# Kernel tuning notes

Measured on AMD Instinct MI355X. Metric: run time of the kernel, lower is better.

The kernel has to match this reference:

```python
import jax, jax.numpy as jnp
import numpy as np
import math

T = 2048; HID = 2048; H = 16; KV = 8; G = H // KV; D = 128
GH = 128; BS = 64; NB = T // BS
EPS = 1e-6; RATIO = 0.2; SCALE = 1.0 / math.sqrt(D)


def _rope_tables(length, dim, theta=1000000.0):
    inv = 1.0 / (theta ** (np.arange(0, dim, 2, dtype=np.float32) / dim))
    f = np.outer(np.arange(length, dtype=np.float32), inv)
    emb = np.concatenate([f, f], axis=-1)
    return jnp.asarray(np.cos(emb)), jnp.asarray(np.sin(emb))


def _rot_half(x):
    d = x.shape[-1] // 2
    return jnp.concatenate([-x[..., d:], x[..., :d]], axis=-1)


def _apply_rope(x, cos, sin):
    # x: [T, nH, D], cos/sin: [T, D] broadcast over head dim
    return x * cos[:, None, :] + _rot_half(x) * sin[:, None, :]


def _rmsnorm(x, w, eps=EPS):
    xf = x.astype(jnp.float32)
    v = jnp.mean(xf * xf, axis=-1, keepdims=True)
    return (w * (xf * jax.lax.rsqrt(v + eps))).astype(x.dtype)


def setup_inputs() -> dict:
    key = jax.random.key(0)
    ks = jax.random.split(key, 8)
    s = 0.02
    hidden_states = jax.random.normal(ks[0], (T, HID), jnp.float32)
    Wq = jax.random.normal(ks[1], (HID, H * D), jnp.float32) * s
    Wk = jax.random.normal(ks[2], (HID, KV * D), jnp.float32) * s
    Wv = jax.random.normal(ks[3], (HID, KV * D), jnp.float32) * s
    Wo = jax.random.normal(ks[4], (H * D, HID), jnp.float32) * s
    q_norm_w = jnp.ones((D,), jnp.float32)
    k_norm_w = jnp.ones((D,), jnp.float32)
    gate_wq = jax.random.normal(ks[5], (D, GH), jnp.float32) * s
    gate_wk = jax.random.normal(ks[6], (D, GH), jnp.float32) * s
    cos, sin = _rope_tables(T, D)
    cos_gq, sin_gq = _rope_tables(T, GH)
    cos_blk, sin_blk = _rope_tables(NB, GH)
    # causal block mask: query t may attend to key block j iff j <= t // BS
    block_attention_mask = (jnp.arange(T)[:, None] // BS) >= jnp.arange(NB)[None, :]
    return dict(hidden_states=hidden_states, Wq=Wq, Wk=Wk, Wv=Wv, Wo=Wo,
                q_norm_w=q_norm_w, k_norm_w=k_norm_w, gate_wq=gate_wq, gate_wk=gate_wk,
                cos=cos, sin=sin, cos_gq=cos_gq, sin_gq=sin_gq,
                cos_blk=cos_blk, sin_blk=sin_blk,
                block_attention_mask=block_attention_mask)


def reference(hidden_states, Wq, Wk, Wv, Wo, q_norm_w, k_norm_w, gate_wq, gate_wk,
              cos, sin, cos_gq, sin_gq, cos_blk, sin_blk, block_attention_mask):
    q = (hidden_states @ Wq).reshape(T, H, D)
    k = (hidden_states @ Wk).reshape(T, KV, D)
    v = (hidden_states @ Wv).reshape(T, KV, D)
    q = _rmsnorm(q, q_norm_w)
    k = _rmsnorm(k, k_norm_w)

    # ---- gate network on un-roped q/k: q-head avg-pool to KV heads, k avg-pool per block ----
    q_pool = q.reshape(T, KV, G, D).mean(axis=2)            # [T, KV, D]
    gq = _apply_rope(q_pool @ gate_wq, cos_gq, sin_gq)      # [T, KV, GH]
    k_blk = k.reshape(NB, BS, KV, D).mean(axis=1)           # [NB, KV, D]
    gk = _apply_rope(k_blk @ gate_wk, cos_blk, sin_blk)     # [NB, KV, GH]
    gate_scores = jnp.einsum('tkg,nkg->ktn', gq, gk) / math.sqrt(GH)  # [KV, T, NB]
    predict_mask = jnp.where(block_attention_mask[None], gate_scores, -1e9)

    # ---- main attention (RoPE + GQA causal softmax attention) ----
    qr = _apply_rope(q, cos, sin)
    kr = _apply_rope(k, cos, sin)
    kr_rep = jnp.repeat(kr, G, axis=1)                      # [T, H, D]
    v_rep = jnp.repeat(v, G, axis=1)
    logits = jnp.einsum('thd,shd->hts', qr, kr_rep) * SCALE  # [H, T, T]
    causal = jnp.tril(jnp.ones((T, T), bool))
    logits = jnp.where(causal[None], logits, -jnp.inf)
    probs = jax.nn.softmax(logits, axis=-1)
    attn_output = jnp.einsum('hts,shd->thd', probs, v_rep).reshape(T, H * D) @ Wo

    # ---- pooled ground-truth block mask: attention mass per key block ----
    pooled = probs.reshape(H, T, NB, BS).sum(axis=-1)        # [H, T, NB]
    gt = pooled.reshape(KV, G, T, NB).max(axis=1)            # max_pool3d over head groups -> [KV,T,NB]
    gt = jnp.where(block_attention_mask[None], gt, 0.0)
    gt = gt / (gt.sum(axis=-1, keepdims=True) + 1e-9)

    # ---- KLDiv gate loss on the tail slice (bsz = 1) ----
    start = int(T * RATIO)
    tgt = gt[:, start:, :]                                   # [KV, L, NB]
    logp = jax.nn.log_softmax(predict_mask[:, start:, :], axis=-1)
    safe_t = jnp.where(tgt > 0, tgt, 1.0)
    kl = jnp.where(tgt > 0, tgt * (jnp.log(safe_t) - logp), 0.0)
    gate_loss = kl.reshape(KV, -1).mean(axis=-1).sum()       # KLDivLoss(reduction='mean') per kv head, summed, /bsz(=1)
    return attn_output, gate_loss
```

## Files before the change

### kernel.cpp

```cpp
#include <hip/hip_runtime.h>

#define T_ 2048
#define HID_ 2048
#define H_ 16
#define KV_ 8
#define G_ 2
#define D_ 128
#define GH_ 128
#define BS_ 64
#define NB_ 32
#define START_ 409
#define TG0_ 384
#define SCALE_ 0.08838834764831845f
#define MFIX_ 8.0f

typedef __attribute__((ext_vector_type(8))) short short8_t;
typedef __attribute__((ext_vector_type(4))) float float4_t;
typedef __attribute__((ext_vector_type(8))) unsigned short ushort8_t;
typedef __attribute__((ext_vector_type(4))) unsigned short ushort4_t;

__device__ __forceinline__ float wave_sum(float v) {
#pragma unroll
  for (int o = 32; o > 0; o >>= 1) v += __shfl_xor(v, o, 64);
  return v;
}
__device__ __forceinline__ unsigned short f2bf(float x) {
  unsigned int u = __float_as_uint(x);
  unsigned int r = (u + 0x7fffu + ((u >> 16) & 1u)) >> 16;
  return (unsigned short)r;
}

__device__ __forceinline__ void gload16(const void* g, void* l) {
  __builtin_amdgcn_global_load_lds((const __attribute__((address_space(1))) unsigned int*)g,
                                   (__attribute__((address_space(3))) unsigned int*)l, 16, 0, 0);
}

__device__ __forceinline__ void castT_dev(const float* __restrict__ in,
                                          unsigned short* __restrict__ out, int K, int N,
                                          int ldin, int bx, int by,
                                          unsigned short (*tile)[72], int tid) {
  int k0 = by * 64, n0 = bx * 64;
  int tx = tid & 63, ty4 = tid >> 6;
#pragma unroll
  for (int i = 0; i < 16; ++i) {
    int ky = ty4 * 16 + i;
    tile[tx][ky] = f2bf(in[(size_t)(k0 + ky) * ldin + n0 + tx]);
  }
  __syncthreads();
#pragma unroll
  for (int i = 0; i < 16; ++i) {
    int ny = ty4 * 16 + i;
    out[(size_t)(n0 + ny) * K + k0 + tx] = tile[ny][tx];
  }
}

__global__ __launch_bounds__(256) void castT(const float* __restrict__ in,
                                             unsigned short* __restrict__ out,
                                             int K, int N, int ldin) {
  __shared__ unsigned short tile[64][72];
  castT_dev(in, out, K, N, ldin, blockIdx.x, blockIdx.y, tile, threadIdx.x);
}

__global__ __launch_bounds__(256) void prep_cast(const float* __restrict__ hs,
                                                 const float* __restrict__ Wq,
                                                 const float* __restrict__ Wk,
                                                 const float* __restrict__ Wv,
                                                 const float* __restrict__ Wo,
                                                 const float* __restrict__ gwq,
                                                 const float* __restrict__ gwk,
                                                 unsigned short* __restrict__ hsb,
                                                 unsigned short* __restrict__ WqkvT,
                                                 unsigned short* __restrict__ WoT,
                                                 unsigned short* __restrict__ gwqT,
                                                 unsigned short* __restrict__ gwkT) {
  __shared__ unsigned short tile[64][72];
  int id = blockIdx.x, tid = threadIdx.x;
  if (id < 4096) {
    int i = id * 256 + tid;
    float4 v = ((const float4*)hs)[i];
    ushort4_t o = {f2bf(v.x), f2bf(v.y), f2bf(v.z), f2bf(v.w)};
    *(ushort4_t*)(hsb + (size_t)i * 4) = o;
  } else if (id < 5120) {
    int t = id - 4096;
    castT_dev(Wq, WqkvT, 2048, 2048, 2048, t & 31, t >> 5, tile, tid);
  } else if (id < 5632) {
    int t = id - 5120;
    castT_dev(Wk, WqkvT + (size_t)2048 * 2048, 2048, 1024, 1024, t & 15, t >> 4, tile, tid);
  } else if (id < 6144) {
    int t = id - 5632;
    castT_dev(Wv, WqkvT + (size_t)3072 * 2048, 2048, 1024, 1024, t & 15, t >> 4, tile, tid);
  } else if (id < 7168) {
    int t = id - 6144;
    castT_dev(Wo, WoT, 2048, 2048, 2048, t & 31, t >> 5, tile, tid);
  } else if (id < 7172) {
    int t = id - 7168;
    castT_dev(gwq, gwqT, 128, 128, 128, t & 1, t >> 1, tile, tid);
  } else {
    int t = id - 7172;
    castT_dev(gwk, gwkT, 128, 128, 128, t & 1, t >> 1, tile, tid);
  }
}

__global__ __launch_bounds__(256) void gemm_bf16_v3(const unsigned short* __restrict__ A,
                                                    const unsigned short* __restrict__ Bt,
                                                    float* __restrict__ C,
                                                    int M, int N, int K, int ldc) {
  __shared__ unsigned short As[128 * 64];
  __shared__ unsigned short Bs[128 * 64];
  int tid = threadIdx.x;
  int wid = tid >> 6, lane = tid & 63;
  int quad = lane >> 4, l16 = lane & 15;
  int wm = wid & 1, wn = wid >> 1;
  int m0 = blockIdx.y * 128, n0 = blockIdx.x * 128;
  const unsigned short* gA[4];
  const unsigned short* gB[4];
#pragma unroll
  for (int it = 0; it < 4; ++it) {
    int line = wid * 32 + it * 8 + (lane >> 3);
    int chunk = (lane & 7) ^ (line & 7);
    gA[it] = A + (size_t)(m0 + line) * K + chunk * 8;
    gB[it] = Bt + (size_t)(n0 + line) * K + chunk * 8;
  }
  float4_t acc[4][4];
#pragma unroll
  for (int i = 0; i < 4; ++i)
#pragma unroll
    for (int j = 0; j < 4; ++j) acc[i][j] = (float4_t){0.f, 0.f, 0.f, 0.f};
  for (int k0 = 0; k0 < K; k0 += 64) {
    __syncthreads();
#pragma unroll
    for (int it = 0; it < 4; ++it) {
      gload16(gA[it] + k0, As + (wid * 32 + it * 8) * 64);
      gload16(gB[it] + k0, Bs + (wid * 32 + it * 8) * 64);
    }
    __syncthreads();
    short8_t a[2][4], b[2][4];
#pragma unroll
    for (int ks = 0; ks < 2; ++ks) {
      int sw = ((ks * 4 + quad) ^ (l16 & 7)) * 8;
#pragma unroll
      for (int i = 0; i < 4; ++i) {
        a[ks][i] = *(const short8_t*)&As[(wm * 64 + i * 16 + l16) * 64 + sw];
        b[ks][i] = *(const short8_t*)&Bs[(wn * 64 + i * 16 + l16) * 64 + sw];
      }
    }
#pragma unroll
    for (int ks = 0; ks < 2; ++ks)
#pragma unroll
      for (int i = 0; i < 4; ++i)
#pragma unroll
        for (int j = 0; j < 4; ++j)
          acc[i][j] = __builtin_amdgcn_mfma_f32_16x16x32_bf16(a[ks][i], b[ks][j], acc[i][j], 0, 0, 0);
  }
#pragma unroll
  for (int i = 0; i < 4; ++i)
#pragma unroll
    for (int j = 0; j < 4; ++j)
#pragma unroll
      for (int reg = 0; reg < 4; ++reg)
        C[(size_t)(m0 + wm * 64 + i * 16 + quad * 4 + reg) * ldc + n0 + wn * 64 + j * 16 + l16] =
            acc[i][j][reg];
}

__global__ __launch_bounds__(128) void norm_rope_fused(const float* __restrict__ qkvf,
                                                       const float* __restrict__ qw,
                                                       const float* __restrict__ kw,
                                                       const float* __restrict__ cosT,
                                                       const float* __restrict__ sinT,
                                                       unsigned short* __restrict__ qbf,
                                                       unsigned short* __restrict__ qpool_bf,
                                                       unsigned short* __restrict__ kbf,
                                                       float* __restrict__ knorm) {
  int t = blockIdx.x, d = threadIdx.x;
  if (blockIdx.y < 8) {
    int kv = blockIdx.y;
    size_t i0 = (size_t)t * 4096 + (kv * G_) * D_ + d;
    float x0 = qkvf[i0], x1 = qkvf[i0 + D_];
    __shared__ float sred[2][2];
    float s0 = wave_sum(x0 * x0), s1 = wave_sum(x1 * x1);
    if ((d & 63) == 0) { sred[0][d >> 6] = s0; sred[1][d >> 6] = s1; }
    __syncthreads();
    float wv = qw[d];
    float n0 = x0 * rsqrtf((sred[0][0] + sred[0][1]) * (1.f / D_) + 1e-6f) * wv;
    float n1 = x1 * rsqrtf((sred[1][0] + sred[1][1]) * (1.f / D_) + 1e-6f) * wv;
    if (t >= TG0_) qpool_bf[((size_t)(t - TG0_) * KV_ + kv) * D_ + d] = f2bf(0.5f * (n0 + n1));
    __shared__ float sh[2][D_];
    sh[0][d] = n0; sh[1][d] = n1;
    __syncthreads();
    float c = cosT[t * D_ + d], s = sinT[t * D_ + d];
    float r0 = (d < 64) ? -sh[0][d + 64] : sh[0][d - 64];
    float r1 = (d < 64) ? -sh[1][d + 64] : sh[1][d - 64];
    qbf[((size_t)(t * H_) + kv * G_) * D_ + d] = f2bf(n0 * c + r0 * s);
    qbf[((size_t)(t * H_) + kv * G_ + 1) * D_ + d] = f2bf(n1 * c + r1 * s);
  } else {
    int kv = blockIdx.y - 8;
    float x = qkvf[(size_t)t * 4096 + 2048 + kv * D_ + d];
    __shared__ float sredk[2];
    float s0 = wave_sum(x * x);
    if ((d & 63) == 0) sredk[d >> 6] = s0;
    __syncthreads();
    float nk = x * rsqrtf((sredk[0] + sredk[1]) * (1.f / D_) + 1e-6f) * kw[d];
    knorm[(size_t)(t * KV_ + kv) * D_ + d] = nk;
    __shared__ float shk[D_];
    shk[d] = nk;
    __syncthreads();
    float rot = (d < 64) ? -shk[d + 64] : shk[d - 64];
    kbf[(size_t)(t * KV_ + kv) * D_ + d] = f2bf(nk * cosT[t * D_ + d] + rot * sinT[t * D_ + d]);
  }
}

__global__ __launch_bounds__(128) void kblk_kernel(const float* __restrict__ knorm,
                                                   unsigned short* __restrict__ kblk_bf) {
  int n = blockIdx.x, kv = blockIdx.y, d = threadIdx.x;
  float s = 0.f;
  for (int i = 0; i < BS_; ++i) s += knorm[((size_t)(n * BS_ + i) * KV_ + kv) * D_ + d];
  kblk_bf[(size_t)(n * KV_ + kv) * D_ + d] = f2bf(s * (1.f / BS_));
}

__global__ __launch_bounds__(128) void rope_g_fused(float* __restrict__ gq, float* __restrict__ gk,
                                                    const float* __restrict__ cosG,
                                                    const float* __restrict__ sinG,
                                                    const float* __restrict__ cosB,
                                                    const float* __restrict__ sinB) {
  int r = blockIdx.x, kvh = blockIdx.y, d = threadIdx.x;
  float* x;
  size_t base;
  float c_, s_;
  if (r < NB_) {
    x = gk;
    base = (size_t)(r * KV_ + kvh) * GH_;
    c_ = cosB[r * GH_ + d]; s_ = sinB[r * GH_ + d];
  } else {
    int rr = r - NB_;
    x = gq;
    base = (size_t)(rr * KV_ + kvh) * GH_;
    c_ = cosG[(size_t)(TG0_ + rr) * GH_ + d]; s_ = sinG[(size_t)(TG0_ + rr) * GH_ + d];
  }
  __shared__ float sh[GH_];
  sh[d] = x[base + d];
  __syncthreads();
  float rot = (d < 64) ? -sh[d + 64] : sh[d - 64];
  x[base + d] = sh[d] * c_ + rot * s_;
}

__global__ __launch_bounds__(256) void attn_mfma(const unsigned short* __restrict__ qbf,
                                                 const unsigned short* __restrict__ kbf,
                                                 const unsigned short* __restrict__ vt,
                                                 unsigned short* __restrict__ attnb,
                                                 float* __restrict__ pooled) {
  int h = blockIdx.x;
  int yy = blockIdx.y;
  int tile = (yy < 16) ? yy : 47 - yy;
  int t0 = tile * 64;
  int tid = threadIdx.x;
  int wid = tid >> 6, lane = tid & 63;
  int quad = lane >> 4, l16 = lane & 15;
  int kv = h >> 1;
  __shared__ unsigned short Ks[2][64 * 128];
  __shared__ unsigned short Vs[2][128 * 64];
  __shared__ unsigned short Ps[4][16 * 72];

  const unsigned short* kbase[4];
  const unsigned short* vbase[4];
#pragma unroll
  for (int it = 0; it < 4; ++it) {
    int seg = wid * 4 + it;
    int krow = seg * 4 + (lane >> 4);
    int kchk = lane & 15;
    kbase[it] = kbf + ((size_t)krow * KV_ + kv) * D_ + ((kchk ^ (krow & 7)) << 3);
    int vrow = seg * 8 + (lane >> 3);
    int vchk = lane & 7;
    vbase[it] = vt + (size_t)(kv * 128 + vrow) * T_ + ((vchk ^ (vrow & 7)) << 3);
  }

  int tq = t0 + wid * 16 + l16;
  short8_t qf[4];
#pragma unroll
  for (int kb = 0; kb < 4; ++kb)
    qf[kb] = *(const short8_t*)&qbf[((size_t)tq * H_ + h) * D_ + kb * 32 + quad * 8];

  const short one_bf = (short)0x3F80;
  short8_t ones = {one_bf, one_bf, one_bf, one_bf, one_bf, one_bf, one_bf, one_bf};

  int tbase = t0 + wid * 16 + quad * 4;
  float l_[4] = {0.f, 0.f, 0.f, 0.f};
  float pacc[2][4] = {};
  float4_t o[8];
#pragma unroll
  for (int j = 0; j < 8; ++j) o[j] = (float4_t){0.f, 0.f, 0.f, 0.f};

  int nchunks = tile + 1;
#pragma unroll
  for (int it = 0; it < 4; ++it) {
    gload16(kbase[it], &Ks[0][(wid * 4 + it) * 512]);
    gload16(vbase[it], &Vs[0][(wid * 4 + it) * 512]);
  }
  for (int c = 0; c < nchunks; ++c) {
    __syncthreads();
    if (c + 1 < nchunks) {
      int b = (c + 1) & 1;
#pragma unroll
      for (int it = 0; it < 4; ++it) {
        gload16(kbase[it] + (size_t)(c + 1) * 65536, &Ks[b][(wid * 4 + it) * 512]);
        gload16(vbase[it] + (c + 1) * 64, &Vs[b][(wid * 4 + it) * 512]);
      }
    }
    const unsigned short* Ksc = Ks[c & 1];
    const unsigned short* Vsc = Vs[c & 1];

    float4_t s[4];
#pragma unroll
    for (int j = 0; j < 4; ++j) {
      float4_t a = (float4_t){0.f, 0.f, 0.f, 0.f};
#pragma unroll
      for (int kb = 0; kb < 4; ++kb) {
        short8_t kf = *(const short8_t*)&Ksc[(j * 16 + l16) * 128 + (((kb * 4 + quad) ^ (l16 & 7)) << 3)];
        a = __builtin_amdgcn_mfma_f32_16x16x32_bf16(qf[kb], kf, a, 0, 0, 0);
      }
      s[j] = a;
    }
    if (c == tile) {
#pragma unroll
      for (int reg = 0; reg < 4; ++reg) {
        int trow = tbase + reg;
#pragma unroll
        for (int j = 0; j < 4; ++j) {
          float p = __expf(s[j][reg] * SCALE_ - MFIX_);
          s[j][reg] = (c * 64 + j * 16 + l16 <= trow) ? p : 0.f;
        }
      }
    } else {
#pragma unroll
      for (int j = 0; j < 4; ++j)
#pragma unroll
        for (int reg = 0; reg < 4; ++reg)
          s[j][reg] = __expf(s[j][reg] * SCALE_ - MFIX_);
    }
#pragma unroll
    for (int j = 0; j < 4; ++j)
#pragma unroll
      for (int reg = 0; reg < 4; ++reg)
        Ps[wid][(quad * 4 + reg) * 72 + j * 16 + l16] = f2bf(s[j][reg]);
    float4_t pool = (float4_t){0.f, 0.f, 0.f, 0.f};
#pragma unroll
    for (int ks = 0; ks < 2; ++ks) {
      short8_t pf = *(const short8_t*)&Ps[wid][l16 * 72 + ks * 32 + quad * 8];
      pool = __builtin_amdgcn_mfma_f32_16x16x32_bf16(pf, ones, pool, 0, 0, 0);
#pragma unroll
      for (int jt = 0; jt < 8; ++jt) {
        short8_t vf = *(const short8_t*)&Vsc[(jt * 16 + l16) * 64 + (((ks * 4 + quad) ^ (l16 & 7)) << 3)];
        o[jt] = __builtin_amdgcn_mfma_f32_16x16x32_bf16(pf, vf, o[jt], 0, 0, 0);
      }
    }
    int half = c >> 4, cl = c & 15;
#pragma unroll
    for (int reg = 0; reg < 4; ++reg) {
      l_[reg] += pool[reg];
      if (l16 == cl) pacc[half][reg] = pool[reg];
    }
  }
  float inv[4];
#pragma unroll
  for (int reg = 0; reg < 4; ++reg) inv[reg] = 1.f / l_[reg];
#pragma unroll
  for (int jt = 0; jt < 8; ++jt)
#pragma unroll
    for (int reg = 0; reg < 4; ++reg)
      attnb[(size_t)(tbase + reg) * (H_ * D_) + h * D_ + jt * 16 + l16] =
          f2bf(o[jt][reg] * inv[reg]);
#pragma unroll
  for (int reg = 0; reg < 4; ++reg) {
    int trow = tbase + reg;
    pooled[((size_t)h * T_ + trow) * NB_ + l16] = pacc[0][reg] * inv[reg];
    pooled[((size_t)h * T_ + trow) * NB_ + 16 + l16] = pacc[1][reg] * inv[reg];
  }
}

__global__ __launch_bounds__(256) void gate_loss2(const float* __restrict__ gq,
                                                  const float* __restrict__ gk,
                                                  const float* __restrict__ pooled,
                                                  float* __restrict__ klsum) {
  int kv = blockIdx.x;
  int sub = threadIdx.x >> 5;
  int n = threadIdx.x & 31;
  int tloc = blockIdx.y * 8 + sub;
  bool act = tloc < (T_ - START_);
  int t = START_ + (act ? tloc : 0);
  const float4* a = (const float4*)(gq + ((size_t)(t - TG0_) * KV_ + kv) * GH_);
  const float4* b = (const float4*)(gk + (size_t)(n * KV_ + kv) * GH_);
  float dot = 0.f;
#pragma unroll
  for (int d4 = 0; d4 < 32; ++d4) {
    float4 av = a[d4], bv = b[d4];
    dot += av.x * bv.x + av.y * bv.y + av.z * bv.z + av.w * bv.w;
  }
  bool valid = (t / BS_) >= n;
  float score = valid ? dot * SCALE_ : -1e9f;
  float M = score;
#pragma unroll
  for (int o = 16; o > 0; o >>= 1) M = fmaxf(M, __shfl_xor(M, o, 64));
  float e = __expf(score - M);
  float Z = e;
#pragma unroll
  for (int o = 16; o > 0; o >>= 1) Z += __shfl_xor(Z, o, 64);
  float logZ = M + logf(Z);
  float g = 0.f;
  if (valid) {
    float p0 = pooled[((size_t)(kv * G_) * T_ + t) * NB_ + n];
    float p1 = pooled[((size_t)(kv * G_ + 1) * T_ + t) * NB_ + n];
    g = fmaxf(p0, p1);
  }
  float gs = g;
#pragma unroll
  for (int o = 16; o > 0; o >>= 1) gs += __shfl_xor(gs, o, 64);
  float tgt = g / (gs + 1e-9f);
  float kl = (tgt > 0.f) ? tgt * (logf(tgt) - (score - logZ)) : 0.f;
  float ks = kl;
#pragma unroll
  for (int o = 16; o > 0; o >>= 1) ks += __shfl_xor(ks, o, 64);
  if (n == 0 && act) klsum[kv * (T_ - START_) + tloc] = ks;
}

__global__ __launch_bounds__(256) void finalize_loss(const float* __restrict__ klsum,
                                                     float* __restrict__ out) {
  const int n = KV_ * (T_ - START_);
  float s = 0.f;
  for (int i = threadIdx.x; i < n; i += 256) s += klsum[i];
  s = wave_sum(s);
  __shared__ float sh[4];
  if ((threadIdx.x & 63) == 0) sh[threadIdx.x >> 6] = s;
  __syncthreads();
  if (threadIdx.x == 0)
    out[0] = (sh[0] + sh[1] + sh[2] + sh[3]) * (1.f / ((float)(T_ - START_) * NB_));
}

extern "C" void kernel_launch(void* const* d_in, const int* in_sizes, int n_in,
                              void* d_out, int out_size, void* d_ws, size_t ws_size,
                              hipStream_t stream) {
  const float* hs   = (const float*)d_in[0];
  const float* Wq   = (const float*)d_in[1];
  const float* Wk   = (const float*)d_in[2];
  const float* Wv   = (const float*)d_in[3];
  const float* Wo   = (const float*)d_in[4];
  const float* qw   = (const float*)d_in[5];
  const float* kw   = (const float*)d_in[6];
  const float* gwq  = (const float*)d_in[7];
  const float* gwk  = (const float*)d_in[8];
  const float* cosT = (const float*)d_in[9];
  const float* sinT = (const float*)d_in[10];
  const float* cosG = (const float*)d_in[11];
  const float* sinG = (const float*)d_in[12];
  const float* cosB = (const float*)d_in[13];
  const float* sinB = (const float*)d_in[14];
  float* out = (float*)d_out;
  float* ws = (float*)d_ws;
  const size_t MEG = 1048576;

  float*          qkvf     = ws;
  unsigned short* attnb    = (unsigned short*)ws;
  float*          pooled   = ws + 2 * MEG;
  float*          klsum    = ws + 3 * MEG;
  unsigned short* WqkvT    = (unsigned short*)(ws + 8 * MEG);
  unsigned short* qbf      = WqkvT;
  unsigned short* kbf      = WqkvT + 4 * MEG;
  unsigned short* vt       = WqkvT + 6 * MEG;
  unsigned short* hsb      = (unsigned short*)(ws + 12 * MEG);
  float*          knorm    = ws + 12 * MEG;
  unsigned short* WoT      = (unsigned short*)(ws + 14 * MEG);
  unsigned short* qpool_bf = (unsigned short*)(ws + 16 * MEG);
  float*          gq       = ws + 17 * MEG;
  unsigned short* kblk_bf  = (unsigned short*)(ws + 18 * MEG + 786432);
  float*          gk       = ws + 18 * MEG + 819200;
  unsigned short* gwqT     = (unsigned short*)(ws + 18 * MEG + 851968);
  unsigned short* gwkT     = (unsigned short*)(ws + 18 * MEG + 860160);

  prep_cast<<<7176, 256, 0, stream>>>(hs, Wq, Wk, Wv, Wo, gwq, gwk, hsb, WqkvT, WoT, gwqT, gwkT);
  gemm_bf16_v3<<<dim3(32, 16), 256, 0, stream>>>(hsb, WqkvT, qkvf, 2048, 4096, 2048, 4096);
  norm_rope_fused<<<dim3(T_, 16), 128, 0, stream>>>(qkvf, qw, kw, cosT, sinT, qbf, qpool_bf,
                                                    kbf, knorm);
  castT<<<dim3(16, 32), 256, 0, stream>>>(qkvf + 3072, vt, T_, 1024, 4096);
  kblk_kernel<<<dim3(NB_, KV_), 128, 0, stream>>>(knorm, kblk_bf);
  gemm_bf16_v3<<<dim3(1, 104), 256, 0, stream>>>(qpool_bf, gwqT, gq, 13312, 128, 128, 128);
  gemm_bf16_v3<<<dim3(1, 2), 256, 0, stream>>>(kblk_bf, gwkT, gk, 256, 128, 128, 128);
  rope_g_fused<<<dim3(NB_ + (T_ - TG0_), KV_), 128, 0, stream>>>(gq, gk, cosG, sinG, cosB, sinB);
  attn_mfma<<<dim3(H_, 32), 256, 0, stream>>>(qbf, kbf, vt, attnb, pooled);
  gemm_bf16_v3<<<dim3(16, 16), 256, 0, stream>>>(attnb, WoT, out, 2048, 2048, 2048, 2048);
  gate_loss2<<<dim3(KV_, 205), 256, 0, stream>>>(gq, gk, pooled, klsum);
  finalize_loss<<<1, 256, 0, stream>>>(klsum, out + (size_t)T_ * HID_);
}
```

Before: 366.7 us.

## Split long causal attention tiles across two blocks with combine kernel

The attention kernel now splits each query tile in the upper half of the sequence into two key-chunk ranges handled by separate blocks, raising the grid from 32 to 48 tiles per head, and adds a combine kernel that sums partial outputs and row sums. It relies on a fixed score max, so partials add without rescaling. Double-buffered K/V loads are replaced by single buffers, which cuts LDS use so four blocks can fit per CU, and the P scratch gets an XOR swizzle in place of padding. Pooled block mass is stored unnormalized and divided by the row sum in the gate-loss kernel, and the two gate GEMMs merge into one launch. The aim is better load balance and occupancy, at the cost of fp32 partial-output traffic, an extra launch and loss of load/compute overlap.

```diff
diff --git a/kernel.cpp b/kernel.cpp
--- a/kernel.cpp
+++ b/kernel.cpp
@@ -101,65 +101,88 @@
   }
 }
 
+__device__ __forceinline__ void gemm_body(const unsigned short* __restrict__ A,
+                                          const unsigned short* __restrict__ Bt,
+                                          float* __restrict__ C,
+                                          int M, int N, int K, int ldc, int bx, int by,
+                                          unsigned short* As, unsigned short* Bs) {
+  int tid = threadIdx.x;
+  int wid = tid >> 6, lane = tid & 63;
+  int quad = lane >> 4, l16 = lane & 15;
+  int wm = wid & 1, wn = wid >> 1;
+  int m0 = by * 128, n0 = bx * 128;
+  const unsigned short* gA[4];
+  const unsigned short* gB[4];
+#pragma unroll
+  for (int it = 0; it < 4; ++it) {
+    int line = wid * 32 + it * 8 + (lane >> 3);
+    int chunk = (lane & 7) ^ (line & 7);
+    gA[it] = A + (size_t)(m0 + line) * K + chunk * 8;
+    gB[it] = Bt + (size_t)(n0 + line) * K + chunk * 8;
+  }
+  float4_t acc[4][4];
+#pragma unroll
+  for (int i = 0; i < 4; ++i)
+#pragma unroll
+    for (int j = 0; j < 4; ++j) acc[i][j] = (float4_t){0.f, 0.f, 0.f, 0.f};
+  for (int k0 = 0; k0 < K; k0 += 64) {
+    __syncthreads();
+#pragma unroll
+    for (int it = 0; it < 4; ++it) {
+      gload16(gA[it] + k0, As + (wid * 32 + it * 8) * 64);
+      gload16(gB[it] + k0, Bs + (wid * 32 + it * 8) * 64);
+    }
+    __syncthreads();
+    short8_t a[2][4], b[2][4];
+#pragma unroll
+    for (int ks = 0; ks < 2; ++ks) {
+      int sw = ((ks * 4 + quad) ^ (l16 & 7)) * 8;
+#pragma unroll
+      for (int i = 0; i < 4; ++i) {
+        a[ks][i] = *(const short8_t*)&As[(wm * 64 + i * 16 + l16) * 64 + sw];
+        b[ks][i] = *(const short8_t*)&Bs[(wn * 64 + i * 16 + l16) * 64 + sw];
+      }
+    }
+#pragma unroll
+    for (int ks = 0; ks < 2; ++ks)
+#pragma unroll
+      for (int i = 0; i < 4; ++i)
+#pragma unroll
+        for (int j = 0; j < 4; ++j)
+          acc[i][j] = __builtin_amdgcn_mfma_f32_16x16x32_bf16(a[ks][i], b[ks][j], acc[i][j], 0, 0, 0);
+  }
+#pragma unroll
+  for (int i = 0; i < 4; ++i)
+#pragma unroll
+    for (int j = 0; j < 4; ++j)
+#pragma unroll
+      for (int reg = 0; reg < 4; ++reg)
+        C[(size_t)(m0 + wm * 64 + i * 16 + quad * 4 + reg) * ldc + n0 + wn * 64 + j * 16 + l16] =
+            acc[i][j][reg];
+}
+
 __global__ __launch_bounds__(256) void gemm_bf16_v3(const unsigned short* __restrict__ A,
                                                     const unsigned short* __restrict__ Bt,
                                                     float* __restrict__ C,
                                                     int M, int N, int K, int ldc) {
   __shared__ unsigned short As[128 * 64];
   __shared__ unsigned short Bs[128 * 64];
-  int tid = threadIdx.x;
-  int wid = tid >> 6, lane = tid & 63;
-  int quad = lane >> 4, l16 = lane & 15;
-  int wm = wid & 1, wn = wid >> 1;
-  int m0 = blockIdx.y * 128, n0 = blockIdx.x * 128;
-  const unsigned short* gA[4];
-  const unsigned short* gB[4];
-#pragma unroll
-  for (int it = 0; it < 4; ++it) {
-    int line = wid * 32 + it * 8 + (lane >> 3);
-    int chunk = (lane & 7) ^ (line & 7);
-    gA[it] = A + (size_t)(m0 + line) * K + chunk * 8;
-    gB[it] = Bt + (size_t)(n0 + line) * K + chunk * 8;
-  }
-  float4_t acc[4][4];
-#pragma unroll
-  for (int i = 0; i < 4; ++i)
-#pragma unroll
-    for (int j = 0; j < 4; ++j) acc[i][j] = (float4_t){0.f, 0.f, 0.f, 0.f};
-  for (int k0 = 0; k0 < K; k0 += 64) {
-    __syncthreads();
-#pragma unroll
-    for (int it = 0; it < 4; ++it) {
-      gload16(gA[it] + k0, As + (wid * 32 + it * 8) * 64);
-      gload16(gB[it] + k0, Bs + (wid * 32 + it * 8) * 64);
-    }
-    __syncthreads();
-    short8_t a[2][4], b[2][4];
-#pragma unroll
-    for (int ks = 0; ks < 2; ++ks) {
-      int sw = ((ks * 4 + quad) ^ (l16 & 7)) * 8;
-#pragma unroll
-      for (int i = 0; i < 4; ++i) {
-        a[ks][i] = *(const short8_t*)&As[(wm * 64 + i * 16 + l16) * 64 + sw];
-        b[ks][i] = *(const short8_t*)&Bs[(wn * 64 + i * 16 + l16) * 64 + sw];
-      }
-    }
-#pragma unroll
-    for (int ks = 0; ks < 2; ++ks)
-#pragma unroll
-      for (int i = 0; i < 4; ++i)
-#pragma unroll
-        for (int j = 0; j < 4; ++j)
-          acc[i][j] = __builtin_amdgcn_mfma_f32_16x16x32_bf16(a[ks][i], b[ks][j], acc[i][j], 0, 0, 0);
-  }
-#pragma unroll
-  for (int i = 0; i < 4; ++i)
-#pragma unroll
-    for (int j = 0; j < 4; ++j)
-#pragma unroll
-      for (int reg = 0; reg < 4; ++reg)
-        C[(size_t)(m0 + wm * 64 + i * 16 + quad * 4 + reg) * ldc + n0 + wn * 64 + j * 16 + l16] =
-            acc[i][j][reg];
+  gemm_body(A, Bt, C, M, N, K, ldc, blockIdx.x, blockIdx.y, As, Bs);
+}
+
+__global__ __launch_bounds__(256) void gemm_gates(const unsigned short* __restrict__ Aq,
+                                                  const unsigned short* __restrict__ Bq,
+                                                  float* __restrict__ Cq,
+                                                  const unsigned short* __restrict__ Ak,
+                                                  const unsigned short* __restrict__ Bk,
+                                                  float* __restrict__ Ck) {
+  __shared__ unsigned short As[128 * 64];
+  __shared__ unsigned short Bs[128 * 64];
+  int y = blockIdx.y;
+  if (y < 104)
+    gemm_body(Aq, Bq, Cq, 13312, 128, 128, 128, 0, y, As, Bs);
+  else
+    gemm_body(Ak, Bk, Ck, 256, 128, 128, 128, 0, y - 104, As, Bs);
 }
 
 __global__ __launch_bounds__(128) void norm_rope_fused(const float* __restrict__ qkvf,
@@ -243,22 +266,29 @@
   x[base + d] = sh[d] * c_ + rot * s_;
 }
 
-__global__ __launch_bounds__(256) void attn_mfma(const unsigned short* __restrict__ qbf,
-                                                 const unsigned short* __restrict__ kbf,
-                                                 const unsigned short* __restrict__ vt,
-                                                 unsigned short* __restrict__ attnb,
-                                                 float* __restrict__ pooled) {
+__global__ __launch_bounds__(256, 4) void attn_mfma(const unsigned short* __restrict__ qbf,
+                                                    const unsigned short* __restrict__ kbf,
+                                                    const unsigned short* __restrict__ vt,
+                                                    unsigned short* __restrict__ attnb,
+                                                    float* __restrict__ pooled,
+                                                    float* __restrict__ o_part0,
+                                                    float* __restrict__ o_part1,
+                                                    float* __restrict__ l_buf,
+                                                    float* __restrict__ l_part1) {
   int h = blockIdx.x;
   int yy = blockIdx.y;
-  int tile = (yy < 16) ? yy : 47 - yy;
+  int tile, c_lo, c_hi;
+  if (yy < 16)      { tile = yy;      c_lo = 0;                c_hi = tile + 1; }
+  else if (yy < 32) { tile = 47 - yy; c_lo = 0;                c_hi = (tile + 2) >> 1; }
+  else              { tile = 63 - yy; c_lo = (tile + 2) >> 1;  c_hi = tile + 1; }
   int t0 = tile * 64;
   int tid = threadIdx.x;
   int wid = tid >> 6, lane = tid & 63;
   int quad = lane >> 4, l16 = lane & 15;
   int kv = h >> 1;
-  __shared__ unsigned short Ks[2][64 * 128];
-  __shared__ unsigned short Vs[2][128 * 64];
-  __shared__ unsigned short Ps[4][16 * 72];
+  __shared__ unsigned short Ks[64 * 128];
+  __shared__ unsigned short Vs[128 * 64];
+  __shared__ unsigned short Ps[4][16 * 64];
 
   const unsigned short* kbase[4];
   const unsigned short* vbase[4];
@@ -289,24 +319,14 @@
 #pragma unroll
   for (int j = 0; j < 8; ++j) o[j] = (float4_t){0.f, 0.f, 0.f, 0.f};
 
-  int nchunks = tile + 1;
-#pragma unroll
-  for (int it = 0; it < 4; ++it) {
-    gload16(kbase[it], &Ks[0][(wid * 4 + it) * 512]);
-    gload16(vbase[it], &Vs[0][(wid * 4 + it) * 512]);
-  }
-  for (int c = 0; c < nchunks; ++c) {
-    __syncthreads();
-    if (c + 1 < nchunks) {
-      int b = (c + 1) & 1;
-#pragma unroll
-      for (int it = 0; it < 4; ++it) {
-        gload16(kbase[it] + (size_t)(c + 1) * 65536, &Ks[b][(wid * 4 + it) * 512]);
-        gload16(vbase[it] + (c + 1) * 64, &Vs[b][(wid * 4 + it) * 512]);
-      }
-    }
-    const unsigned short* Ksc = Ks[c & 1];
-    const unsigned short* Vsc = Vs[c & 1];
+  for (int c = c_lo; c < c_hi; ++c) {
+    __syncthreads();
+#pragma unroll
+    for (int it = 0; it < 4; ++it) {
+      gload16(kbase[it] + (size_t)c * 65536, &Ks[(wid * 4 + it) * 512]);
+      gload16(vbase[it] + c * 64, &Vs[(wid * 4 + it) * 512]);
+    }
+    __syncthreads();
 
     float4_t s[4];
 #pragma unroll
@@ -314,7 +334,7 @@
       float4_t a = (float4_t){0.f, 0.f, 0.f, 0.f};
 #pragma unroll
       for (int kb = 0; kb < 4; ++kb) {
-        short8_t kf = *(const short8_t*)&Ksc[(j * 16 + l16) * 128 + (((kb * 4 + quad) ^ (l16 & 7)) << 3)];
+        short8_t kf = *(const short8_t*)&Ks[(j * 16 + l16) * 128 + (((kb * 4 + quad) ^ (l16 & 7)) << 3)];
         a = __builtin_amdgcn_mfma_f32_16x16x32_bf16(qf[kb], kf, a, 0, 0, 0);
       }
       s[j] = a;
@@ -339,16 +359,18 @@
 #pragma unroll
     for (int j = 0; j < 4; ++j)
 #pragma unroll
-      for (int reg = 0; reg < 4; ++reg)
-        Ps[wid][(quad * 4 + reg) * 72 + j * 16 + l16] = f2bf(s[j][reg]);
+      for (int reg = 0; reg < 4; ++reg) {
+        int r = quad * 4 + reg;
+        Ps[wid][r * 64 + ((j * 16 + l16) ^ ((r & 7) << 3))] = f2bf(s[j][reg]);
+      }
     float4_t pool = (float4_t){0.f, 0.f, 0.f, 0.f};
 #pragma unroll
     for (int ks = 0; ks < 2; ++ks) {
-      short8_t pf = *(const short8_t*)&Ps[wid][l16 * 72 + ks * 32 + quad * 8];
+      short8_t pf = *(const short8_t*)&Ps[wid][l16 * 64 + (((ks * 4 + quad) ^ (l16 & 7)) << 3)];
       pool = __builtin_amdgcn_mfma_f32_16x16x32_bf16(pf, ones, pool, 0, 0, 0);
 #pragma unroll
       for (int jt = 0; jt < 8; ++jt) {
-        short8_t vf = *(const short8_t*)&Vsc[(jt * 16 + l16) * 64 + (((ks * 4 + quad) ^ (l16 & 7)) << 3)];
+        short8_t vf = *(const short8_t*)&Vs[(jt * 16 + l16) * 64 + (((ks * 4 + quad) ^ (l16 & 7)) << 3)];
         o[jt] = __builtin_amdgcn_mfma_f32_16x16x32_bf16(pf, vf, o[jt], 0, 0, 0);
       }
     }
@@ -359,26 +381,72 @@
       if (l16 == cl) pacc[half][reg] = pool[reg];
     }
   }
-  float inv[4];
-#pragma unroll
-  for (int reg = 0; reg < 4; ++reg) inv[reg] = 1.f / l_[reg];
-#pragma unroll
-  for (int jt = 0; jt < 8; ++jt)
-#pragma unroll
-    for (int reg = 0; reg < 4; ++reg)
-      attnb[(size_t)(tbase + reg) * (H_ * D_) + h * D_ + jt * 16 + l16] =
-          f2bf(o[jt][reg] * inv[reg]);
 #pragma unroll
   for (int reg = 0; reg < 4; ++reg) {
     int trow = tbase + reg;
-    pooled[((size_t)h * T_ + trow) * NB_ + l16] = pacc[0][reg] * inv[reg];
-    pooled[((size_t)h * T_ + trow) * NB_ + 16 + l16] = pacc[1][reg] * inv[reg];
-  }
+    if (l16 >= c_lo && l16 < c_hi)
+      pooled[((size_t)h * T_ + trow) * NB_ + l16] = pacc[0][reg];
+    if (16 + l16 >= c_lo && 16 + l16 < c_hi)
+      pooled[((size_t)h * T_ + trow) * NB_ + 16 + l16] = pacc[1][reg];
+  }
+  if (yy < 16) {
+    float inv[4];
+#pragma unroll
+    for (int reg = 0; reg < 4; ++reg) inv[reg] = 1.f / l_[reg];
+#pragma unroll
+    for (int jt = 0; jt < 8; ++jt)
+#pragma unroll
+      for (int reg = 0; reg < 4; ++reg)
+        attnb[(size_t)(tbase + reg) * (H_ * D_) + h * D_ + jt * 16 + l16] =
+            f2bf(o[jt][reg] * inv[reg]);
+    if (l16 == 0) {
+#pragma unroll
+      for (int reg = 0; reg < 4; ++reg) l_buf[(size_t)h * T_ + tbase + reg] = l_[reg];
+    }
+  } else {
+    float* ob = (yy < 32) ? o_part0 : o_part1;
+    size_t rb = (size_t)h * 1024 + (size_t)(tbase - 1024);
+#pragma unroll
+    for (int jt = 0; jt < 8; ++jt)
+#pragma unroll
+      for (int reg = 0; reg < 4; ++reg)
+        ob[(rb + reg) * 128 + jt * 16 + l16] = o[jt][reg];
+    if (l16 == 0) {
+      if (yy < 32) {
+#pragma unroll
+        for (int reg = 0; reg < 4; ++reg) l_buf[(size_t)h * T_ + tbase + reg] = l_[reg];
+      } else {
+#pragma unroll
+        for (int reg = 0; reg < 4; ++reg) l_part1[rb + reg] = l_[reg];
+      }
+    }
+  }
+}
+
+__global__ __launch_bounds__(256) void attn_combine(const float* __restrict__ o0,
+                                                    const float* __restrict__ o1,
+                                                    const float* __restrict__ l1p,
+                                                    unsigned short* __restrict__ attnb,
+                                                    float* __restrict__ l_buf) {
+  int gid = blockIdx.x * 256 + threadIdx.x;
+  int row = gid >> 5, q4 = gid & 31;
+  int h = row >> 10, tt = row & 1023;
+  float la = l_buf[(size_t)h * T_ + 1024 + tt];
+  float lb = l1p[row];
+  float lt = la + lb;
+  float inv = 1.f / lt;
+  float4 a = ((const float4*)o0)[gid];
+  float4 b = ((const float4*)o1)[gid];
+  ushort4_t ov = {f2bf((a.x + b.x) * inv), f2bf((a.y + b.y) * inv),
+                  f2bf((a.z + b.z) * inv), f2bf((a.w + b.w) * inv)};
+  *(ushort4_t*)(attnb + (size_t)(1024 + tt) * (H_ * D_) + h * D_ + q4 * 4) = ov;
+  if (q4 == 0) l_buf[(size_t)h * T_ + 1024 + tt] = lt;
 }
 
 __global__ __launch_bounds__(256) void gate_loss2(const float* __restrict__ gq,
                                                   const float* __restrict__ gk,
                                                   const float* __restrict__ pooled,
+                                                  const float* __restrict__ l_buf,
                                                   float* __restrict__ klsum) {
   int kv = blockIdx.x;
   int sub = threadIdx.x >> 5;
@@ -406,8 +474,10 @@
   float logZ = M + logf(Z);
   float g = 0.f;
   if (valid) {
-    float p0 = pooled[((size_t)(kv * G_) * T_ + t) * NB_ + n];
-    float p1 = pooled[((size_t)(kv * G_ + 1) * T_ + t) * NB_ + n];
+    float rl0 = 1.f / l_buf[(size_t)(kv * G_) * T_ + t];
+    float rl1 = 1.f / l_buf[(size_t)(kv * G_ + 1) * T_ + t];
+    float p0 = pooled[((size_t)(kv * G_) * T_ + t) * NB_ + n] * rl0;
+    float p1 = pooled[((size_t)(kv * G_ + 1) * T_ + t) * NB_ + n] * rl1;
     g = fmaxf(p0, p1);
   }
   float gs = g;
@@ -460,6 +530,10 @@
   unsigned short* attnb    = (unsigned short*)ws;
   float*          pooled   = ws + 2 * MEG;
   float*          klsum    = ws + 3 * MEG;
+  float*          l_buf    = ws + 3 * MEG + 65536;
+  float*          l_part1  = ws + 3 * MEG + 98304;
+  float*          o_part0  = ws + 4 * MEG;
+  float*          o_part1  = ws + 6 * MEG;
   unsigned short* WqkvT    = (unsigned short*)(ws + 8 * MEG);
   unsigned short* qbf      = WqkvT;
   unsigned short* kbf      = WqkvT + 4 * MEG;
@@ -480,11 +554,12 @@
                                                     kbf, knorm);
   castT<<<dim3(16, 32), 256, 0, stream>>>(qkvf + 3072, vt, T_, 1024, 4096);
   kblk_kernel<<<dim3(NB_, KV_), 128, 0, stream>>>(knorm, kblk_bf);
-  gemm_bf16_v3<<<dim3(1, 104), 256, 0, stream>>>(qpool_bf, gwqT, gq, 13312, 128, 128, 128);
-  gemm_bf16_v3<<<dim3(1, 2), 256, 0, stream>>>(kblk_bf, gwkT, gk, 256, 128, 128, 128);
+  gemm_gates<<<dim3(1, 106), 256, 0, stream>>>(qpool_bf, gwqT, gq, kblk_bf, gwkT, gk);
   rope_g_fused<<<dim3(NB_ + (T_ - TG0_), KV_), 128, 0, stream>>>(gq, gk, cosG, sinG, cosB, sinB);
-  attn_mfma<<<dim3(H_, 32), 256, 0, stream>>>(qbf, kbf, vt, attnb, pooled);
+  attn_mfma<<<dim3(H_, 48), 256, 0, stream>>>(qbf, kbf, vt, attnb, pooled, o_part0, o_part1,
+                                              l_buf, l_part1);
+  attn_combine<<<2048, 256, 0, stream>>>(o_part0, o_part1, l_part1, attnb, l_buf);
   gemm_bf16_v3<<<dim3(16, 16), 256, 0, stream>>>(attnb, WoT, out, 2048, 2048, 2048, 2048);
-  gate_loss2<<<dim3(KV_, 205), 256, 0, stream>>>(gq, gk, pooled, klsum);
+  gate_loss2<<<dim3(KV_, 205), 256, 0, stream>>>(gq, gk, pooled, l_buf, klsum);
   finalize_loss<<<1, 256, 0, stream>>>(klsum, out + (size_t)T_ * HID_);
 }
```

Measured after the change: 366.4 us. Within noise of the previous version (-0.1%).

## Split attention KV range across blocks, share K/V between GQA heads, merge gate GEMMs

Applied to the files above, without the earlier changes.

The attention kernel now processes both query heads of a KV group in one block, so K/V tiles loaded into shared memory are reused twice. Each query tile's key range is split into two halves handled by separate blocks, with partial outputs and row sums combined through float atomics and a new combine kernel that normalizes and casts to bf16. The two small gate GEMMs are merged into one launch. In exchange the kernel holds more registers (launch bounds set to 2 blocks per CU), and the change adds atomic traffic, two memsets, an extra pass over a 16 MB fp32 buffer, and nondeterministic summation order.

```diff
diff --git a/kernel.cpp b/kernel.cpp
--- a/kernel.cpp
+++ b/kernel.cpp
@@ -101,65 +101,88 @@
   }
 }
 
+__device__ __forceinline__ void gemm_body(const unsigned short* __restrict__ A,
+                                          const unsigned short* __restrict__ Bt,
+                                          float* __restrict__ C,
+                                          int M, int N, int K, int ldc, int bx, int by,
+                                          unsigned short* As, unsigned short* Bs) {
+  int tid = threadIdx.x;
+  int wid = tid >> 6, lane = tid & 63;
+  int quad = lane >> 4, l16 = lane & 15;
+  int wm = wid & 1, wn = wid >> 1;
+  int m0 = by * 128, n0 = bx * 128;
+  const unsigned short* gA[4];
+  const unsigned short* gB[4];
+#pragma unroll
+  for (int it = 0; it < 4; ++it) {
+    int line = wid * 32 + it * 8 + (lane >> 3);
+    int chunk = (lane & 7) ^ (line & 7);
+    gA[it] = A + (size_t)(m0 + line) * K + chunk * 8;
+    gB[it] = Bt + (size_t)(n0 + line) * K + chunk * 8;
+  }
+  float4_t acc[4][4];
+#pragma unroll
+  for (int i = 0; i < 4; ++i)
+#pragma unroll
+    for (int j = 0; j < 4; ++j) acc[i][j] = (float4_t){0.f, 0.f, 0.f, 0.f};
+  for (int k0 = 0; k0 < K; k0 += 64) {
+    __syncthreads();
+#pragma unroll
+    for (int it = 0; it < 4; ++it) {
+      gload16(gA[it] + k0, As + (wid * 32 + it * 8) * 64);
+      gload16(gB[it] + k0, Bs + (wid * 32 + it * 8) * 64);
+    }
+    __syncthreads();
+    short8_t a[2][4], b[2][4];
+#pragma unroll
+    for (int ks = 0; ks < 2; ++ks) {
+      int sw = ((ks * 4 + quad) ^ (l16 & 7)) * 8;
+#pragma unroll
+      for (int i = 0; i < 4; ++i) {
+        a[ks][i] = *(const short8_t*)&As[(wm * 64 + i * 16 + l16) * 64 + sw];
+        b[ks][i] = *(const short8_t*)&Bs[(wn * 64 + i * 16 + l16) * 64 + sw];
+      }
+    }
+#pragma unroll
+    for (int ks = 0; ks < 2; ++ks)
+#pragma unroll
+      for (int i = 0; i < 4; ++i)
+#pragma unroll
+        for (int j = 0; j < 4; ++j)
+          acc[i][j] = __builtin_amdgcn_mfma_f32_16x16x32_bf16(a[ks][i], b[ks][j], acc[i][j], 0, 0, 0);
+  }
+#pragma unroll
+  for (int i = 0; i < 4; ++i)
+#pragma unroll
+    for (int j = 0; j < 4; ++j)
+#pragma unroll
+      for (int reg = 0; reg < 4; ++reg)
+        C[(size_t)(m0 + wm * 64 + i * 16 + quad * 4 + reg) * ldc + n0 + wn * 64 + j * 16 + l16] =
+            acc[i][j][reg];
+}
+
 __global__ __launch_bounds__(256) void gemm_bf16_v3(const unsigned short* __restrict__ A,
                                                     const unsigned short* __restrict__ Bt,
                                                     float* __restrict__ C,
                                                     int M, int N, int K, int ldc) {
   __shared__ unsigned short As[128 * 64];
   __shared__ unsigned short Bs[128 * 64];
-  int tid = threadIdx.x;
-  int wid = tid >> 6, lane = tid & 63;
-  int quad = lane >> 4, l16 = lane & 15;
-  int wm = wid & 1, wn = wid >> 1;
-  int m0 = blockIdx.y * 128, n0 = blockIdx.x * 128;
-  const unsigned short* gA[4];
-  const unsigned short* gB[4];
-#pragma unroll
-  for (int it = 0; it < 4; ++it) {
-    int line = wid * 32 + it * 8 + (lane >> 3);
-    int chunk = (lane & 7) ^ (line & 7);
-    gA[it] = A + (size_t)(m0 + line) * K + chunk * 8;
-    gB[it] = Bt + (size_t)(n0 + line) * K + chunk * 8;
-  }
-  float4_t acc[4][4];
-#pragma unroll
-  for (int i = 0; i < 4; ++i)
-#pragma unroll
-    for (int j = 0; j < 4; ++j) acc[i][j] = (float4_t){0.f, 0.f, 0.f, 0.f};
-  for (int k0 = 0; k0 < K; k0 += 64) {
-    __syncthreads();
-#pragma unroll
-    for (int it = 0; it < 4; ++it) {
-      gload16(gA[it] + k0, As + (wid * 32 + it * 8) * 64);
-      gload16(gB[it] + k0, Bs + (wid * 32 + it * 8) * 64);
-    }
-    __syncthreads();
-    short8_t a[2][4], b[2][4];
-#pragma unroll
-    for (int ks = 0; ks < 2; ++ks) {
-      int sw = ((ks * 4 + quad) ^ (l16 & 7)) * 8;
-#pragma unroll
-      for (int i = 0; i < 4; ++i) {
-        a[ks][i] = *(const short8_t*)&As[(wm * 64 + i * 16 + l16) * 64 + sw];
-        b[ks][i] = *(const short8_t*)&Bs[(wn * 64 + i * 16 + l16) * 64 + sw];
-      }
-    }
-#pragma unroll
-    for (int ks = 0; ks < 2; ++ks)
-#pragma unroll
-      for (int i = 0; i < 4; ++i)
-#pragma unroll
-        for (int j = 0; j < 4; ++j)
-          acc[i][j] = __builtin_amdgcn_mfma_f32_16x16x32_bf16(a[ks][i], b[ks][j], acc[i][j], 0, 0, 0);
-  }
-#pragma unroll
-  for (int i = 0; i < 4; ++i)
-#pragma unroll
-    for (int j = 0; j < 4; ++j)
-#pragma unroll
-      for (int reg = 0; reg < 4; ++reg)
-        C[(size_t)(m0 + wm * 64 + i * 16 + quad * 4 + reg) * ldc + n0 + wn * 64 + j * 16 + l16] =
-            acc[i][j][reg];
+  gemm_body(A, Bt, C, M, N, K, ldc, blockIdx.x, blockIdx.y, As, Bs);
+}
+
+__global__ __launch_bounds__(256) void gemm_gates(const unsigned short* __restrict__ Aq,
+                                                  const unsigned short* __restrict__ Bq,
+                                                  float* __restrict__ Cq,
+                                                  const unsigned short* __restrict__ Ak,
+                                                  const unsigned short* __restrict__ Bk,
+                                                  float* __restrict__ Ck) {
+  __shared__ unsigned short As[128 * 64];
+  __shared__ unsigned short Bs[128 * 64];
+  int y = blockIdx.y;
+  if (y < 104)
+    gemm_body(Aq, Bq, Cq, 13312, 128, 128, 128, 0, y, As, Bs);
+  else
+    gemm_body(Ak, Bk, Ck, 256, 128, 128, 128, 0, y - 104, As, Bs);
 }
 
 __global__ __launch_bounds__(128) void norm_rope_fused(const float* __restrict__ qkvf,
@@ -243,19 +266,21 @@
   x[base + d] = sh[d] * c_ + rot * s_;
 }
 
-__global__ __launch_bounds__(256) void attn_mfma(const unsigned short* __restrict__ qbf,
-                                                 const unsigned short* __restrict__ kbf,
-                                                 const unsigned short* __restrict__ vt,
-                                                 unsigned short* __restrict__ attnb,
-                                                 float* __restrict__ pooled) {
-  int h = blockIdx.x;
+__global__ __launch_bounds__(256, 2) void attn_mfma(const unsigned short* __restrict__ qbf,
+                                                    const unsigned short* __restrict__ kbf,
+                                                    const unsigned short* __restrict__ vt,
+                                                    float* __restrict__ pooled,
+                                                    float* __restrict__ o_acc,
+                                                    float* __restrict__ l_acc) {
+  int kv = blockIdx.x;
   int yy = blockIdx.y;
-  int tile = (yy < 16) ? yy : 47 - yy;
+  int tile, c_lo, c_hi;
+  if (yy < 32) { tile = yy;      c_lo = 0;                c_hi = (tile + 2) >> 1; }
+  else         { tile = 63 - yy; c_lo = (tile + 2) >> 1;  c_hi = tile + 1; }
   int t0 = tile * 64;
   int tid = threadIdx.x;
   int wid = tid >> 6, lane = tid & 63;
   int quad = lane >> 4, l16 = lane & 15;
-  int kv = h >> 1;
   __shared__ unsigned short Ks[2][64 * 128];
   __shared__ unsigned short Vs[2][128 * 64];
   __shared__ unsigned short Ps[4][16 * 72];
@@ -274,30 +299,33 @@
   }
 
   int tq = t0 + wid * 16 + l16;
-  short8_t qf[4];
-#pragma unroll
-  for (int kb = 0; kb < 4; ++kb)
-    qf[kb] = *(const short8_t*)&qbf[((size_t)tq * H_ + h) * D_ + kb * 32 + quad * 8];
+  short8_t qf[2][4];
+#pragma unroll
+  for (int hh = 0; hh < 2; ++hh)
+#pragma unroll
+    for (int kb = 0; kb < 4; ++kb)
+      qf[hh][kb] = *(const short8_t*)&qbf[((size_t)tq * H_ + kv * G_ + hh) * D_ + kb * 32 + quad * 8];
 
   const short one_bf = (short)0x3F80;
   short8_t ones = {one_bf, one_bf, one_bf, one_bf, one_bf, one_bf, one_bf, one_bf};
 
   int tbase = t0 + wid * 16 + quad * 4;
-  float l_[4] = {0.f, 0.f, 0.f, 0.f};
-  float pacc[2][4] = {};
-  float4_t o[8];
-#pragma unroll
-  for (int j = 0; j < 8; ++j) o[j] = (float4_t){0.f, 0.f, 0.f, 0.f};
-
-  int nchunks = tile + 1;
+  float l_[2][4] = {};
+  float pacc[2][2][4] = {};
+  float4_t o[2][8];
+#pragma unroll
+  for (int hh = 0; hh < 2; ++hh)
+#pragma unroll
+    for (int j = 0; j < 8; ++j) o[hh][j] = (float4_t){0.f, 0.f, 0.f, 0.f};
+
 #pragma unroll
   for (int it = 0; it < 4; ++it) {
-    gload16(kbase[it], &Ks[0][(wid * 4 + it) * 512]);
-    gload16(vbase[it], &Vs[0][(wid * 4 + it) * 512]);
-  }
-  for (int c = 0; c < nchunks; ++c) {
-    __syncthreads();
-    if (c + 1 < nchunks) {
+    gload16(kbase[it] + (size_t)c_lo * 65536, &Ks[c_lo & 1][(wid * 4 + it) * 512]);
+    gload16(vbase[it] + c_lo * 64, &Vs[c_lo & 1][(wid * 4 + it) * 512]);
+  }
+  for (int c = c_lo; c < c_hi; ++c) {
+    __syncthreads();
+    if (c + 1 < c_hi) {
       int b = (c + 1) & 1;
 #pragma unroll
       for (int it = 0; it < 4; ++it) {
@@ -307,78 +335,101 @@
     }
     const unsigned short* Ksc = Ks[c & 1];
     const unsigned short* Vsc = Vs[c & 1];
-
-    float4_t s[4];
-#pragma unroll
-    for (int j = 0; j < 4; ++j) {
-      float4_t a = (float4_t){0.f, 0.f, 0.f, 0.f};
-#pragma unroll
-      for (int kb = 0; kb < 4; ++kb) {
-        short8_t kf = *(const short8_t*)&Ksc[(j * 16 + l16) * 128 + (((kb * 4 + quad) ^ (l16 & 7)) << 3)];
-        a = __builtin_amdgcn_mfma_f32_16x16x32_bf16(qf[kb], kf, a, 0, 0, 0);
+    int half = c >> 4, cl = c & 15;
+
+#pragma unroll
+    for (int hh = 0; hh < 2; ++hh) {
+      float4_t s[4];
+#pragma unroll
+      for (int j = 0; j < 4; ++j) {
+        float4_t a = (float4_t){0.f, 0.f, 0.f, 0.f};
+#pragma unroll
+        for (int kb = 0; kb < 4; ++kb) {
+          short8_t kf = *(const short8_t*)&Ksc[(j * 16 + l16) * 128 + (((kb * 4 + quad) ^ (l16 & 7)) << 3)];
+          a = __builtin_amdgcn_mfma_f32_16x16x32_bf16(qf[hh][kb], kf, a, 0, 0, 0);
+        }
+        s[j] = a;
       }
-      s[j] = a;
-    }
-    if (c == tile) {
-#pragma unroll
-      for (int reg = 0; reg < 4; ++reg) {
-        int trow = tbase + reg;
-#pragma unroll
-        for (int j = 0; j < 4; ++j) {
-          float p = __expf(s[j][reg] * SCALE_ - MFIX_);
-          s[j][reg] = (c * 64 + j * 16 + l16 <= trow) ? p : 0.f;
+      if (c == tile) {
+#pragma unroll
+        for (int reg = 0; reg < 4; ++reg) {
+          int trow = tbase + reg;
+#pragma unroll
+          for (int j = 0; j < 4; ++j) {
+            float p = __expf(s[j][reg] * SCALE_ - MFIX_);
+            s[j][reg] = (c * 64 + j * 16 + l16 <= trow) ? p : 0.f;
+          }
+        }
+      } else {
+#pragma unroll
+        for (int j = 0; j < 4; ++j)
+#pragma unroll
+          for (int reg = 0; reg < 4; ++reg)
+            s[j][reg] = __expf(s[j][reg] * SCALE_ - MFIX_);
+      }
+#pragma unroll
+      for (int j = 0; j < 4; ++j)
+#pragma unroll
+        for (int reg = 0; reg < 4; ++reg)
+          Ps[wid][(quad * 4 + reg) * 72 + j * 16 + l16] = f2bf(s[j][reg]);
+      float4_t pool = (float4_t){0.f, 0.f, 0.f, 0.f};
+#pragma unroll
+      for (int ks = 0; ks < 2; ++ks) {
+        short8_t pf = *(const short8_t*)&Ps[wid][l16 * 72 + ks * 32 + quad * 8];
+        pool = __builtin_amdgcn_mfma_f32_16x16x32_bf16(pf, ones, pool, 0, 0, 0);
+#pragma unroll
+        for (int jt = 0; jt < 8; ++jt) {
+          short8_t vf = *(const short8_t*)&Vsc[(jt * 16 + l16) * 64 + (((ks * 4 + quad) ^ (l16 & 7)) << 3)];
+          o[hh][jt] = __builtin_amdgcn_mfma_f32_16x16x32_bf16(pf, vf, o[hh][jt], 0, 0, 0);
         }
       }
-    } else {
-#pragma unroll
-      for (int j = 0; j < 4; ++j)
-#pragma unroll
-        for (int reg = 0; reg < 4; ++reg)
-          s[j][reg] = __expf(s[j][reg] * SCALE_ - MFIX_);
-    }
-#pragma unroll
-    for (int j = 0; j < 4; ++j)
-#pragma unroll
-      for (int reg = 0; reg < 4; ++reg)
-        Ps[wid][(quad * 4 + reg) * 72 + j * 16 + l16] = f2bf(s[j][reg]);
-    float4_t pool = (float4_t){0.f, 0.f, 0.f, 0.f};
-#pragma unroll
-    for (int ks = 0; ks < 2; ++ks) {
-      short8_t pf = *(const short8_t*)&Ps[wid][l16 * 72 + ks * 32 + quad * 8];
-      pool = __builtin_amdgcn_mfma_f32_16x16x32_bf16(pf, ones, pool, 0, 0, 0);
-#pragma unroll
-      for (int jt = 0; jt < 8; ++jt) {
-        short8_t vf = *(const short8_t*)&Vsc[(jt * 16 + l16) * 64 + (((ks * 4 + quad) ^ (l16 & 7)) << 3)];
-        o[jt] = __builtin_amdgcn_mfma_f32_16x16x32_bf16(pf, vf, o[jt], 0, 0, 0);
+#pragma unroll
+      for (int reg = 0; reg < 4; ++reg) {
+        l_[hh][reg] += pool[reg];
+        if (l16 == cl) pacc[hh][half][reg] = pool[reg];
       }
     }
-    int half = c >> 4, cl = c & 15;
+  }
+#pragma unroll
+  for (int hh = 0; hh < 2; ++hh) {
+    int h = kv * G_ + hh;
 #pragma unroll
     for (int reg = 0; reg < 4; ++reg) {
-      l_[reg] += pool[reg];
-      if (l16 == cl) pacc[half][reg] = pool[reg];
+      int trow = tbase + reg;
+      if (l16 >= c_lo && l16 < c_hi)
+        pooled[((size_t)h * T_ + trow) * NB_ + l16] = pacc[hh][0][reg];
+      if (16 + l16 >= c_lo && 16 + l16 < c_hi)
+        pooled[((size_t)h * T_ + trow) * NB_ + 16 + l16] = pacc[hh][1][reg];
     }
-  }
-  float inv[4];
-#pragma unroll
-  for (int reg = 0; reg < 4; ++reg) inv[reg] = 1.f / l_[reg];
-#pragma unroll
-  for (int jt = 0; jt < 8; ++jt)
-#pragma unroll
-    for (int reg = 0; reg < 4; ++reg)
-      attnb[(size_t)(tbase + reg) * (H_ * D_) + h * D_ + jt * 16 + l16] =
-          f2bf(o[jt][reg] * inv[reg]);
-#pragma unroll
-  for (int reg = 0; reg < 4; ++reg) {
-    int trow = tbase + reg;
-    pooled[((size_t)h * T_ + trow) * NB_ + l16] = pacc[0][reg] * inv[reg];
-    pooled[((size_t)h * T_ + trow) * NB_ + 16 + l16] = pacc[1][reg] * inv[reg];
-  }
+#pragma unroll
+    for (int jt = 0; jt < 8; ++jt)
+#pragma unroll
+      for (int reg = 0; reg < 4; ++reg)
+        atomicAdd(&o_acc[(((size_t)h * T_) + tbase + reg) * D_ + jt * 16 + l16], o[hh][jt][reg]);
+    if (l16 == 0) {
+#pragma unroll
+      for (int reg = 0; reg < 4; ++reg)
+        atomicAdd(&l_acc[(size_t)h * T_ + tbase + reg], l_[hh][reg]);
+    }
+  }
+}
+
+__global__ __launch_bounds__(256) void attn_combine(const float* __restrict__ o_acc,
+                                                    const float* __restrict__ l_acc,
+                                                    unsigned short* __restrict__ attnb) {
+  int gid = blockIdx.x * 256 + threadIdx.x;
+  int row = gid >> 5, q4 = gid & 31;
+  int h = row >> 11, t = row & 2047;
+  float inv = 1.f / l_acc[row];
+  float4 a = ((const float4*)o_acc)[gid];
+  ushort4_t ov = {f2bf(a.x * inv), f2bf(a.y * inv), f2bf(a.z * inv), f2bf(a.w * inv)};
+  *(ushort4_t*)(attnb + (size_t)t * (H_ * D_) + h * D_ + q4 * 4) = ov;
 }
 
 __global__ __launch_bounds__(256) void gate_loss2(const float* __restrict__ gq,
                                                   const float* __restrict__ gk,
                                                   const float* __restrict__ pooled,
+                                                  const float* __restrict__ l_acc,
                                                   float* __restrict__ klsum) {
   int kv = blockIdx.x;
   int sub = threadIdx.x >> 5;
@@ -406,8 +457,10 @@
   float logZ = M + logf(Z);
   float g = 0.f;
   if (valid) {
-    float p0 = pooled[((size_t)(kv * G_) * T_ + t) * NB_ + n];
-    float p1 = pooled[((size_t)(kv * G_ + 1) * T_ + t) * NB_ + n];
+    float rl0 = 1.f / l_acc[(size_t)(kv * G_) * T_ + t];
+    float rl1 = 1.f / l_acc[(size_t)(kv * G_ + 1) * T_ + t];
+    float p0 = pooled[((size_t)(kv * G_) * T_ + t) * NB_ + n] * rl0;
+    float p1 = pooled[((size_t)(kv * G_ + 1) * T_ + t) * NB_ + n] * rl1;
     g = fmaxf(p0, p1);
   }
   float gs = g;
@@ -460,6 +513,8 @@
   unsigned short* attnb    = (unsigned short*)ws;
   float*          pooled   = ws + 2 * MEG;
   float*          klsum    = ws + 3 * MEG;
+  float*          l_acc    = ws + 3 * MEG + 65536;
+  float*          o_acc    = ws + 4 * MEG;
   unsigned short* WqkvT    = (unsigned short*)(ws + 8 * MEG);
   unsigned short* qbf      = WqkvT;
   unsigned short* kbf      = WqkvT + 4 * MEG;
@@ -479,12 +534,14 @@
   norm_rope_fused<<<dim3(T_, 16), 128, 0, stream>>>(qkvf, qw, kw, cosT, sinT, qbf, qpool_bf,
                                                     kbf, knorm);
   castT<<<dim3(16, 32), 256, 0, stream>>>(qkvf + 3072, vt, T_, 1024, 4096);
+  hipMemsetAsync(o_acc, 0, (size_t)4 * MEG * sizeof(float), stream);
+  hipMemsetAsync(l_acc, 0, (size_t)H_ * T_ * sizeof(float), stream);
   kblk_kernel<<<dim3(NB_, KV_), 128, 0, stream>>>(knorm, kblk_bf);
-  gemm_bf16_v3<<<dim3(1, 104), 256, 0, stream>>>(qpool_bf, gwqT, gq, 13312, 128, 128, 128);
-  gemm_bf16_v3<<<dim3(1, 2), 256, 0, stream>>>(kblk_bf, gwkT, gk, 256, 128, 128, 128);
+  gemm_gates<<<dim3(1, 106), 256, 0, stream>>>(qpool_bf, gwqT, gq, kblk_bf, gwkT, gk);
   rope_g_fused<<<dim3(NB_ + (T_ - TG0_), KV_), 128, 0, stream>>>(gq, gk, cosG, sinG, cosB, sinB);
-  attn_mfma<<<dim3(H_, 32), 256, 0, stream>>>(qbf, kbf, vt, attnb, pooled);
+  attn_mfma<<<dim3(KV_, 64), 256, 0, stream>>>(qbf, kbf, vt, pooled, o_acc, l_acc);
+  attn_combine<<<4096, 256, 0, stream>>>(o_acc, l_acc, attnb);
   gemm_bf16_v3<<<dim3(16, 16), 256, 0, stream>>>(attnb, WoT, out, 2048, 2048, 2048, 2048);
-  gate_loss2<<<dim3(KV_, 205), 256, 0, stream>>>(gq, gk, pooled, klsum);
+  gate_loss2<<<dim3(KV_, 205), 256, 0, stream>>>(gq, gk, pooled, l_acc, klsum);
   finalize_loss<<<1, 256, 0, stream>>>(klsum, out + (size_t)T_ * HID_);
 }
```

After: 360.0 us. About the same (-1.8%).
